# Kernel optimization log

Hardware: AMD Instinct MI355X
Metric: run time of the kernel (lower is better)

The kernel has to match this reference:

```python
import jax, jax.numpy as jnp
import numpy as np
from jax import lax

B, T, H, CTX, CONV_OUT = 32, 1536, 1024, 1024, 32


def setup_inputs() -> dict:
    key = jax.random.key(0)
    ks = jax.random.split(key, 10)
    s = 1.0 / np.sqrt(H)
    return {
        "decoder_output": jax.random.normal(ks[0], (B, 1, H), jnp.float32),
        "encoder_outputs": jax.random.normal(ks[1], (B, T, H), jnp.float32),
        "last_alignment": jax.random.uniform(ks[2], (B, T), jnp.float32),
        "W": jax.random.normal(ks[3], (CTX, H), jnp.float32) * s,
        "V": jax.random.normal(ks[4], (CTX, H), jnp.float32) * s,
        "U": jax.random.normal(ks[5], (CTX, CONV_OUT), jnp.float32) * (1.0 / np.sqrt(CONV_OUT)),
        "b": jax.random.uniform(ks[6], (CTX,), jnp.float32, -0.1, 0.1),
        "w": jax.random.normal(ks[7], (CTX,), jnp.float32) * (1.0 / np.sqrt(CTX)),
        "conv_w": jax.random.normal(ks[8], (CONV_OUT, 1, 3), jnp.float32) * 0.5,
        "conv_b": jax.random.normal(ks[9], (CONV_OUT,), jnp.float32) * 0.1,
    }


def reference(decoder_output, encoder_outputs, last_alignment, W, V, U, b, w, conv_w, conv_b):
    # location feature: Conv1d(1 -> conv_out, k=3, pad=1) over previous alignment
    conv = lax.conv_general_dilated(
        last_alignment[:, None, :], conv_w,
        window_strides=(1,), padding=[(1, 1)],
        dimension_numbers=("NCW", "OIW", "NCW"),
    ) + conv_b[None, :, None]                      # (B, conv_out, T)
    loc = jnp.transpose(conv, (0, 2, 1))           # (B, T, conv_out)

    # additive (Bahdanau) energies: (B,1,ctx) + (B,T,ctx) + (B,T,ctx) + (ctx,)
    e = jnp.tanh(
        jnp.einsum("bqh,ch->bqc", decoder_output, W)
        + jnp.einsum("bth,ch->btc", encoder_outputs, V)
        + jnp.einsum("btk,ck->btc", loc, U)
        + b
    )                                              # (B, T, ctx)
    scores = jnp.einsum("btc,c->bt", e, w)         # (B, T)
    alignment = jax.nn.softmax(scores, axis=-1)    # (B, T)
    context = jnp.einsum("bt,bth->bh", alignment, encoder_outputs)  # (B, H)
    return context, alignment
```

## Files before the change

kernel.cpp:

```cpp
#include <hip/hip_runtime.h>
#include <hip/hip_bf16.h>
#include <hip/hip_fp16.h>


constexpr int kB = 32, kT = 1536, kH = 1024, kC = 1024, kCO = 32;
constexpr int kM = kB * kT;
constexpr int kKp = 1088;

typedef _Float16 f16;
typedef _Float16 f16x8 __attribute__((ext_vector_type(8)));
typedef float f32x4 __attribute__((ext_vector_type(4)));

constexpr size_t W2_A     = 0;
constexpr size_t W2_B     = W2_A + (size_t)kM * kKp * 2;
constexpr size_t W2_ADD   = W2_B + (size_t)kC * kKp * 2;
constexpr size_t W2_SCORE = W2_ADD + (size_t)kB * kC * 4;
constexpr size_t W2_CTXP  = W2_SCORE + (size_t)8 * kM * 4;

__device__ __forceinline__ void gload16(const void* g, void* l) {
    __builtin_amdgcn_global_load_lds(
        (const __attribute__((address_space(1))) void*)g,
        (__attribute__((address_space(3))) void*)l, 16, 0, 0);
}

__global__ void k_cvt(const float* __restrict__ enc, f16* __restrict__ Af) {
    int gid = blockIdx.x * 256 + threadIdx.x;
    int row = gid >> 7, c8 = gid & 127;
    const float* src = enc + (size_t)row * kH + c8 * 8;
    float4 e0 = *(const float4*)src;
    float4 e1 = *(const float4*)(src + 4);
    union { f16 h[8]; int4 q; } u;
    u.h[0] = (f16)e0.x; u.h[1] = (f16)e0.y; u.h[2] = (f16)e0.z; u.h[3] = (f16)e0.w;
    u.h[4] = (f16)e1.x; u.h[5] = (f16)e1.y; u.h[6] = (f16)e1.z; u.h[7] = (f16)e1.w;
    *(int4*)(Af + (size_t)row * kKp + c8 * 8) = u.q;
}

__global__ void k_loc(const float* __restrict__ la, const float* __restrict__ cw,
                      const float* __restrict__ cb, f16* __restrict__ Af) {
    int m = blockIdx.x * 256 + threadIdx.x;
    int b = m / kT, t = m - b * kT;
    float x0 = (t > 0)      ? la[(size_t)b * kT + t - 1] : 0.f;
    float x1 = la[(size_t)b * kT + t];
    float x2 = (t < kT - 1) ? la[(size_t)b * kT + t + 1] : 0.f;
    union { f16 h[32]; int4 q[4]; } u;
#pragma unroll
    for (int k = 0; k < 32; ++k)
        u.h[k] = (f16)(cw[k * 3] * x0 + cw[k * 3 + 1] * x1 + cw[k * 3 + 2] * x2 + cb[k]);
    int4* dst = (int4*)(Af + (size_t)m * kKp + kH);
    dst[0] = u.q[0]; dst[1] = u.q[1]; dst[2] = u.q[2]; dst[3] = u.q[3];
    int4 z = {0, 0, 0, 0};
    dst[4] = z; dst[5] = z; dst[6] = z; dst[7] = z;
}

__global__ void k_prep_b2(const float* __restrict__ V, const float* __restrict__ U,
                          f16* __restrict__ Bf) {
    int c = blockIdx.x;
    for (int k = threadIdx.x; k < kKp; k += 256) {
        float v = (k < kH) ? V[(size_t)c * kH + k]
                : (k < kH + kCO) ? U[(size_t)c * kCO + (k - kH)] : 0.f;
        Bf[(size_t)c * kKp + k] = (f16)v;
    }
}

__global__ void k_prep_add(const float* __restrict__ dec, const float* __restrict__ W,
                           const float* __restrict__ bias, float* __restrict__ add) {
    __shared__ float dl[kH];
    int bb = blockIdx.x >> 2;
    int cc = (blockIdx.x & 3) * 256 + threadIdx.x;
    *(float4*)&dl[threadIdx.x * 4] = *(const float4*)&dec[(size_t)bb * kH + threadIdx.x * 4];
    __syncthreads();
    float acc = bias[cc];
    const float* wr = W + (size_t)cc * kH;
    for (int h = 0; h < kH; h += 4) {
        float4 wv = *(const float4*)&wr[h];
        acc += wv.x * dl[h] + wv.y * dl[h + 1] + wv.z * dl[h + 2] + wv.w * dl[h + 3];
    }
    add[(size_t)bb * kC + cc] = acc;
}

__launch_bounds__(256, 4)
__global__ void k_main(const f16* __restrict__ Ag, const f16* __restrict__ Bg,
                       const float* __restrict__ add, const float* __restrict__ wvec,
                       float* __restrict__ spart) {
    __shared__ __align__(16) char smem[34816];
    float* add_l = (float*)(smem + 32768);
    float* w_l   = (float*)(smem + 33280);
    float (*sred)[64][2] = (float (*)[64][2])(smem + 33792);

    const int tid = threadIdx.x, lane = tid & 63, wave = tid >> 6;
    const int wm = wave >> 1, wn = wave & 1;
    const int raw = blockIdx.x;
    const int lin = (raw & 7) * 384 + (raw >> 3);
    const int mt = lin >> 3, nt = lin & 7;
    const int m0 = mt * 128, n0 = nt * 128;
    const int bb = m0 / kT;

    if (tid < 128) {
        add_l[tid] = add[(size_t)bb * kC + n0 + tid];
        w_l[tid]   = wvec[n0 + tid];
    }

    f32x4 acc[4][4];
#pragma unroll
    for (int i = 0; i < 4; ++i)
#pragma unroll
        for (int j = 0; j < 4; ++j) acc[i][j] = (f32x4){0.f, 0.f, 0.f, 0.f};

    const int rG = lane >> 3;
    const int gc = (lane & 7) ^ (rG & 7);
    const f16* aS[4]; const f16* bS[4];
#pragma unroll
    for (int j = 0; j < 4; ++j) {
        aS[j] = Ag + (size_t)(m0 + wave * 32 + j * 8 + rG) * kKp + gc * 8;
        bS[j] = Bg + (size_t)(n0 + wave * 32 + j * 8 + rG) * kKp + gc * 8;
    }
    const unsigned aDst = wave * 4096u;
    const unsigned bDst = 16384u + wave * 4096u;
    const int g = lane >> 4, rl = lane & 15;

    for (int t = 0; t < 17; ++t) {
#pragma unroll
        for (int j = 0; j < 4; ++j) gload16(aS[j] + t * 64, smem + aDst + j * 1024);
#pragma unroll
        for (int j = 0; j < 4; ++j) gload16(bS[j] + t * 64, smem + bDst + j * 1024);
        __syncthreads();
#pragma unroll
        for (int kk = 0; kk < 2; ++kk) {
            f16x8 bfv[4], af[4];
#pragma unroll
            for (int ni = 0; ni < 4; ++ni)
                bfv[ni] = *(const f16x8*)(smem + 16384 + (wn * 64 + ni * 16 + rl) * 128
                                          + (((kk * 4 + g) ^ (rl & 7)) << 4));
#pragma unroll
            for (int mi = 0; mi < 4; ++mi)
                af[mi] = *(const f16x8*)(smem + (wm * 64 + mi * 16 + rl) * 128
                                         + (((kk * 4 + g) ^ (rl & 7)) << 4));
            __builtin_amdgcn_s_setprio(1);
#pragma unroll
            for (int mi = 0; mi < 4; ++mi)
#pragma unroll
                for (int ni = 0; ni < 4; ++ni)
                    acc[mi][ni] = __builtin_amdgcn_mfma_f32_16x16x32_f16(af[mi], bfv[ni], acc[mi][ni], 0, 0, 0);
            __builtin_amdgcn_s_setprio(0);
        }
        __syncthreads();
    }

#pragma unroll
    for (int mi = 0; mi < 4; ++mi) {
#pragma unroll
        for (int i = 0; i < 4; ++i) {
            float p = 0.f;
#pragma unroll
            for (int ni = 0; ni < 4; ++ni) {
                int cl = wn * 64 + ni * 16 + rl;
                float e = tanhf(acc[mi][ni][i] + add_l[cl]);
                p += e * w_l[cl];
            }
            p += __shfl_xor(p, 1);
            p += __shfl_xor(p, 2);
            p += __shfl_xor(p, 4);
            p += __shfl_xor(p, 8);
            if (rl == 0) sred[wm][mi * 16 + g * 4 + i][wn] = p;
        }
    }
    __syncthreads();
    if (tid < 128) {
        int r = tid & 63, w2 = tid >> 6;
        float s = sred[w2][r][0] + sred[w2][r][1];
        spart[(size_t)nt * kM + m0 + tid] = s;
    }
}

__global__ void k_softmax(const float* __restrict__ spart, float* __restrict__ out_align) {
    __shared__ float red[256];
    int b = blockIdx.x, tid = threadIdx.x;
    float v[6];
    float mx = -1e30f;
#pragma unroll
    for (int i = 0; i < 6; ++i) {
        size_t idx = (size_t)b * kT + tid + i * 256;
        float s = 0.f;
#pragma unroll
        for (int p = 0; p < 8; ++p) s += spart[(size_t)p * kM + idx];
        v[i] = s; mx = fmaxf(mx, s);
    }
    red[tid] = mx; __syncthreads();
    for (int o = 128; o > 0; o >>= 1) { if (tid < o) red[tid] = fmaxf(red[tid], red[tid + o]); __syncthreads(); }
    mx = red[0]; __syncthreads();
    float sum = 0.f;
#pragma unroll
    for (int i = 0; i < 6; ++i) { v[i] = expf(v[i] - mx); sum += v[i]; }
    red[tid] = sum; __syncthreads();
    for (int o = 128; o > 0; o >>= 1) { if (tid < o) red[tid] += red[tid + o]; __syncthreads(); }
    float inv = 1.f / red[0];
#pragma unroll
    for (int i = 0; i < 6; ++i)
        out_align[(size_t)b * kT + tid + i * 256] = v[i] * inv;
}

__global__ void k_ctx_part(const f16* __restrict__ Af, const float* __restrict__ align,
                           float* __restrict__ cpart) {
    __shared__ float al[192];
    int ci = blockIdx.x, b = blockIdx.y, tid = threadIdx.x;
    if (tid < 192) al[tid] = align[(size_t)b * kT + ci * 192 + tid];
    __syncthreads();
    float4 acc = {0.f, 0.f, 0.f, 0.f};
    const f16* ep = Af + ((size_t)b * kT + (size_t)ci * 192) * kKp + tid * 4;
    for (int t = 0; t < 192; ++t) {
        float a = al[t];
        f16 e0 = ep[(size_t)t * kKp + 0], e1 = ep[(size_t)t * kKp + 1];
        f16 e2 = ep[(size_t)t * kKp + 2], e3 = ep[(size_t)t * kKp + 3];
        acc.x += a * (float)e0; acc.y += a * (float)e1;
        acc.z += a * (float)e2; acc.w += a * (float)e3;
    }
    *(float4*)&cpart[((size_t)ci * kB + b) * kH + tid * 4] = acc;
}

__global__ void k_ctx_red(const float* __restrict__ cpart, float* __restrict__ out_ctx) {
    int idx = blockIdx.x * 256 + threadIdx.x;
    float s = 0.f;
#pragma unroll
    for (int ci = 0; ci < 8; ++ci) s += cpart[(size_t)ci * kB * kH + idx];
    out_ctx[idx] = s;
}

extern "C" void kernel_launch(void* const* d_in, const int* in_sizes, int n_in,
                              void* d_out, int out_size, void* d_ws, size_t ws_size,
                              hipStream_t stream) {
    const float* dec  = (const float*)d_in[0];
    const float* enc  = (const float*)d_in[1];
    const float* la   = (const float*)d_in[2];
    const float* W    = (const float*)d_in[3];
    const float* V    = (const float*)d_in[4];
    const float* U    = (const float*)d_in[5];
    const float* bias = (const float*)d_in[6];
    const float* wv   = (const float*)d_in[7];
    const float* cw   = (const float*)d_in[8];
    const float* cb   = (const float*)d_in[9];

    char* ws = (char*)d_ws;
    f16* Af      = (f16*)(ws + W2_A);
    f16* Bf      = (f16*)(ws + W2_B);
    float* add   = (float*)(ws + W2_ADD);
    float* spart = (float*)(ws + W2_SCORE);
    float* cpart = (float*)(ws + W2_CTXP);

    float* out_ctx   = (float*)d_out;
    float* out_align = (float*)d_out + kB * kH;

    hipLaunchKernelGGL(k_prep_b2,  dim3(kC),             dim3(256), 0, stream, V, U, Bf);
    hipLaunchKernelGGL(k_loc,      dim3(kM / 256),       dim3(256), 0, stream, la, cw, cb, Af);
    hipLaunchKernelGGL(k_cvt,      dim3(kM * kH / 8 / 256), dim3(256), 0, stream, enc, Af);
    hipLaunchKernelGGL(k_prep_add, dim3(kB * 4),         dim3(256), 0, stream, dec, W, bias, add);
    hipLaunchKernelGGL(k_main,     dim3((kM / 128) * 8), dim3(256), 0, stream, Af, Bf, add, wv, spart);
    hipLaunchKernelGGL(k_softmax,  dim3(kB),             dim3(256), 0, stream, spart, out_align);
    hipLaunchKernelGGL(k_ctx_part, dim3(8, kB),          dim3(256), 0, stream, Af, out_align, cpart);
    hipLaunchKernelGGL(k_ctx_red,  dim3(kB * kH / 256),  dim3(256), 0, stream, cpart, out_ctx);
}
```

Measured before the change: 239.6 us.

## Double-buffer GEMM K loop, vectorize weight prep and context partial sums

The main GEMM kernel now loads K-chunks of 32 into two alternating LDS buffers, prefetching the next chunk while MFMAs run on the current one. This removes one of the two barriers per iteration and hides global-to-LDS latency, at the cost of twice as many loop iterations and a new swizzle. The weight-prep kernel now converts 8 values per thread with vector loads. The context partial-sum kernel reads f16x8 vectors and splits time across two halves, producing 16 partials instead of 8. The score and context scratch buffers now share workspace memory.

```diff
diff --git a/kernel.cpp b/kernel.cpp
--- a/kernel.cpp
+++ b/kernel.cpp
@@ -11,11 +11,10 @@
 typedef _Float16 f16x8 __attribute__((ext_vector_type(8)));
 typedef float f32x4 __attribute__((ext_vector_type(4)));
 
-constexpr size_t W2_A     = 0;
-constexpr size_t W2_B     = W2_A + (size_t)kM * kKp * 2;
-constexpr size_t W2_ADD   = W2_B + (size_t)kC * kKp * 2;
-constexpr size_t W2_SCORE = W2_ADD + (size_t)kB * kC * 4;
-constexpr size_t W2_CTXP  = W2_SCORE + (size_t)8 * kM * 4;
+constexpr size_t W2_A    = 0;
+constexpr size_t W2_B    = W2_A + (size_t)kM * kKp * 2;
+constexpr size_t W2_ADD  = W2_B + (size_t)kC * kKp * 2;
+constexpr size_t W2_SCR  = W2_ADD + (size_t)kB * kC * 4;
 
 __device__ __forceinline__ void gload16(const void* g, void* l) {
     __builtin_amdgcn_global_load_lds(
@@ -54,12 +53,23 @@
 
 __global__ void k_prep_b2(const float* __restrict__ V, const float* __restrict__ U,
                           f16* __restrict__ Bf) {
-    int c = blockIdx.x;
-    for (int k = threadIdx.x; k < kKp; k += 256) {
-        float v = (k < kH) ? V[(size_t)c * kH + k]
-                : (k < kH + kCO) ? U[(size_t)c * kCO + (k - kH)] : 0.f;
-        Bf[(size_t)c * kKp + k] = (f16)v;
-    }
+    int c = blockIdx.x, k8 = threadIdx.x;
+    if (k8 >= 136) return;
+    union { f16 h[8]; int4 q; } u;
+    if (k8 < 128) {
+        const float* src = V + (size_t)c * kH + k8 * 8;
+        float4 a = *(const float4*)src, b = *(const float4*)(src + 4);
+        u.h[0] = (f16)a.x; u.h[1] = (f16)a.y; u.h[2] = (f16)a.z; u.h[3] = (f16)a.w;
+        u.h[4] = (f16)b.x; u.h[5] = (f16)b.y; u.h[6] = (f16)b.z; u.h[7] = (f16)b.w;
+    } else if (k8 < 132) {
+        const float* src = U + (size_t)c * kCO + (k8 - 128) * 8;
+        float4 a = *(const float4*)src, b = *(const float4*)(src + 4);
+        u.h[0] = (f16)a.x; u.h[1] = (f16)a.y; u.h[2] = (f16)a.z; u.h[3] = (f16)a.w;
+        u.h[4] = (f16)b.x; u.h[5] = (f16)b.y; u.h[6] = (f16)b.z; u.h[7] = (f16)b.w;
+    } else {
+        u.q = (int4){0, 0, 0, 0};
+    }
+    *(int4*)(Bf + (size_t)c * kKp + k8 * 8) = u.q;
 }
 
 __global__ void k_prep_add(const float* __restrict__ dec, const float* __restrict__ W,
@@ -106,44 +116,55 @@
 #pragma unroll
         for (int j = 0; j < 4; ++j) acc[i][j] = (f32x4){0.f, 0.f, 0.f, 0.f};
 
-    const int rG = lane >> 3;
-    const int gc = (lane & 7) ^ (rG & 7);
-    const f16* aS[4]; const f16* bS[4];
-#pragma unroll
-    for (int j = 0; j < 4; ++j) {
-        aS[j] = Ag + (size_t)(m0 + wave * 32 + j * 8 + rG) * kKp + gc * 8;
-        bS[j] = Bg + (size_t)(n0 + wave * 32 + j * 8 + rG) * kKp + gc * 8;
-    }
-    const unsigned aDst = wave * 4096u;
-    const unsigned bDst = 16384u + wave * 4096u;
+    const int SRl  = lane >> 3;
+    const int slot = (lane & 7) ^ SRl;
+    const int scol = (slot & 3) * 8;
+    const int sr0  = 2 * (wave * 16 + SRl) + (slot >> 2);
+    const int sr1  = 2 * (wave * 16 + 8 + SRl) + (slot >> 2);
+    const f16* aS0 = Ag + (size_t)(m0 + sr0) * kKp + scol;
+    const f16* aS1 = Ag + (size_t)(m0 + sr1) * kKp + scol;
+    const f16* bS0 = Bg + (size_t)(n0 + sr0) * kKp + scol;
+    const f16* bS1 = Bg + (size_t)(n0 + sr1) * kKp + scol;
+    const unsigned aDst = wave * 2048u;
+    const unsigned bDst = 8192u + wave * 2048u;
+
     const int g = lane >> 4, rl = lane & 15;
-
-    for (int t = 0; t < 17; ++t) {
-#pragma unroll
-        for (int j = 0; j < 4; ++j) gload16(aS[j] + t * 64, smem + aDst + j * 1024);
-#pragma unroll
-        for (int j = 0; j < 4; ++j) gload16(bS[j] + t * 64, smem + bDst + j * 1024);
+    const unsigned phys = (unsigned)((((rl & 1) << 2) + g) ^ (rl >> 1));
+    const unsigned aRd = (unsigned)((wm * 32 + (rl >> 1)) * 128) + phys * 16u;
+    const unsigned bRd = 8192u + (unsigned)((wn * 32 + (rl >> 1)) * 128) + phys * 16u;
+
+    gload16(aS0, smem + aDst);
+    gload16(aS1, smem + aDst + 1024);
+    gload16(bS0, smem + bDst);
+    gload16(bS1, smem + bDst + 1024);
+    __syncthreads();
+
+    unsigned bufC = 0u;
+    for (int t = 0; t < 34; ++t) {
+        if (t < 33) {
+            const int o = (t + 1) * 32;
+            const unsigned bn = bufC ^ 16384u;
+            gload16(aS0 + o, smem + bn + aDst);
+            gload16(aS1 + o, smem + bn + aDst + 1024);
+            gload16(bS0 + o, smem + bn + bDst);
+            gload16(bS1 + o, smem + bn + bDst + 1024);
+        }
+        f16x8 af[4], bfv[4];
+#pragma unroll
+        for (int ni = 0; ni < 4; ++ni)
+            bfv[ni] = *(const f16x8*)(smem + bufC + bRd + ni * 1024);
+#pragma unroll
+        for (int mi = 0; mi < 4; ++mi)
+            af[mi] = *(const f16x8*)(smem + bufC + aRd + mi * 1024);
+        __builtin_amdgcn_s_setprio(1);
+#pragma unroll
+        for (int mi = 0; mi < 4; ++mi)
+#pragma unroll
+            for (int ni = 0; ni < 4; ++ni)
+                acc[mi][ni] = __builtin_amdgcn_mfma_f32_16x16x32_f16(af[mi], bfv[ni], acc[mi][ni], 0, 0, 0);
+        __builtin_amdgcn_s_setprio(0);
         __syncthreads();
-#pragma unroll
-        for (int kk = 0; kk < 2; ++kk) {
-            f16x8 bfv[4], af[4];
-#pragma unroll
-            for (int ni = 0; ni < 4; ++ni)
-                bfv[ni] = *(const f16x8*)(smem + 16384 + (wn * 64 + ni * 16 + rl) * 128
-                                          + (((kk * 4 + g) ^ (rl & 7)) << 4));
-#pragma unroll
-            for (int mi = 0; mi < 4; ++mi)
-                af[mi] = *(const f16x8*)(smem + (wm * 64 + mi * 16 + rl) * 128
-                                         + (((kk * 4 + g) ^ (rl & 7)) << 4));
-            __builtin_amdgcn_s_setprio(1);
-#pragma unroll
-            for (int mi = 0; mi < 4; ++mi)
-#pragma unroll
-                for (int ni = 0; ni < 4; ++ni)
-                    acc[mi][ni] = __builtin_amdgcn_mfma_f32_16x16x32_f16(af[mi], bfv[ni], acc[mi][ni], 0, 0, 0);
-            __builtin_amdgcn_s_setprio(0);
-        }
-        __syncthreads();
+        bufC ^= 16384u;
     }
 
 #pragma unroll
@@ -205,23 +226,26 @@
     int ci = blockIdx.x, b = blockIdx.y, tid = threadIdx.x;
     if (tid < 192) al[tid] = align[(size_t)b * kT + ci * 192 + tid];
     __syncthreads();
-    float4 acc = {0.f, 0.f, 0.f, 0.f};
-    const f16* ep = Af + ((size_t)b * kT + (size_t)ci * 192) * kKp + tid * 4;
-    for (int t = 0; t < 192; ++t) {
-        float a = al[t];
-        f16 e0 = ep[(size_t)t * kKp + 0], e1 = ep[(size_t)t * kKp + 1];
-        f16 e2 = ep[(size_t)t * kKp + 2], e3 = ep[(size_t)t * kKp + 3];
-        acc.x += a * (float)e0; acc.y += a * (float)e1;
-        acc.z += a * (float)e2; acc.w += a * (float)e3;
-    }
-    *(float4*)&cpart[((size_t)ci * kB + b) * kH + tid * 4] = acc;
+    const int half = tid >> 7;
+    const int c8 = tid & 127;
+    float a0 = 0.f, a1 = 0.f, a2 = 0.f, a3 = 0.f, a4 = 0.f, a5 = 0.f, a6 = 0.f, a7 = 0.f;
+    const f16* ep = Af + ((size_t)b * kT + ci * 192 + half * 96) * kKp + c8 * 8;
+    for (int t = 0; t < 96; ++t) {
+        float a = al[half * 96 + t];
+        f16x8 e = *(const f16x8*)(ep + (size_t)t * kKp);
+        a0 += a * (float)e[0]; a1 += a * (float)e[1]; a2 += a * (float)e[2]; a3 += a * (float)e[3];
+        a4 += a * (float)e[4]; a5 += a * (float)e[5]; a6 += a * (float)e[6]; a7 += a * (float)e[7];
+    }
+    size_t base = ((size_t)(ci * 2 + half) * kB + b) * kH + (size_t)c8 * 8;
+    *(float4*)&cpart[base]     = (float4){a0, a1, a2, a3};
+    *(float4*)&cpart[base + 4] = (float4){a4, a5, a6, a7};
 }
 
 __global__ void k_ctx_red(const float* __restrict__ cpart, float* __restrict__ out_ctx) {
     int idx = blockIdx.x * 256 + threadIdx.x;
     float s = 0.f;
 #pragma unroll
-    for (int ci = 0; ci < 8; ++ci) s += cpart[(size_t)ci * kB * kH + idx];
+    for (int p = 0; p < 16; ++p) s += cpart[(size_t)p * kB * kH + idx];
     out_ctx[idx] = s;
 }
 
@@ -243,8 +267,8 @@
     f16* Af      = (f16*)(ws + W2_A);
     f16* Bf      = (f16*)(ws + W2_B);
     float* add   = (float*)(ws + W2_ADD);
-    float* spart = (float*)(ws + W2_SCORE);
-    float* cpart = (float*)(ws + W2_CTXP);
+    float* spart = (float*)(ws + W2_SCR);
+    float* cpart = (float*)(ws + W2_SCR);
 
     float* out_ctx   = (float*)d_out;
     float* out_align = (float*)d_out + kB * kH;
```

Measured after the change: 254.7 us. 6.3% more time.
